# Kernel optimization log

Hardware: AMD Instinct MI355X
Metric: run time of the kernel (lower is better)

Reference implementation:

```python
import jax, jax.numpy as jnp
import numpy as np

N = 100000
E = 1600000
IN_FT = 128
OUT_FT = 128
SELF_LOOP_FILL = 3.0


def setup_inputs() -> dict:
    key = jax.random.key(0)
    k1, k2, k3, k4 = jax.random.split(key, 4)
    seq = jax.random.normal(k1, (N, IN_FT), dtype=jnp.float32)
    edge_index = jax.random.randint(k2, (2, E), 0, N, dtype=jnp.int64)
    edge_weight = jax.random.uniform(k3, (E,), dtype=jnp.float32)
    # xavier_uniform for Linear(in_ft, out_ft): W shape [out_ft, in_ft]
    limit = float(np.sqrt(6.0 / (IN_FT + OUT_FT)))
    W = jax.random.uniform(k4, (OUT_FT, IN_FT), dtype=jnp.float32, minval=-limit, maxval=limit)
    return {"seq": seq, "edge_weight": edge_weight, "W": W, "edge_index": edge_index}


def reference(seq, edge_weight, W, edge_index):
    n = seq.shape[0]
    # dropout with drop_prob=0.0 is identity; fc_1: x = seq @ W^T
    x = seq @ W.T  # [N, out_ft]
    # add self loops with fill_value=3.0
    loops = jnp.arange(n, dtype=edge_index.dtype)
    row = jnp.concatenate([edge_index[0], loops])
    col = jnp.concatenate([edge_index[1], loops])
    w = jnp.concatenate([edge_weight, jnp.full((n,), SELF_LOOP_FILL, dtype=edge_weight.dtype)])
    # symmetric normalization: deg^-1/2 [row] * w * deg^-1/2 [col]
    deg = jax.ops.segment_sum(w, row, num_segments=n)
    deg_inv_sqrt = jnp.where(deg > 0, jax.lax.rsqrt(deg), jnp.zeros_like(deg))
    norm = deg_inv_sqrt[row] * w * deg_inv_sqrt[col]
    # sparse aggregation: out[r] += norm_e * x[c]
    out = jax.ops.segment_sum(norm[:, None] * x[col], row, num_segments=n)
    return jax.nn.relu(out)
```

## Files before the change

kernel.cpp:

```cpp
#include <hip/hip_runtime.h>


#define TPB 256
#define NBROWS 256
#define BCAP 4608
#define RCAP 48
#define EPB 8192

typedef __attribute__((ext_vector_type(8))) short s16x8;
typedef __attribute__((ext_vector_type(4))) float f32x4;

__global__ void k_init(int* __restrict__ cursor, int m) {
    int i = blockIdx.x * TPB + threadIdx.x;
    if (i < m) cursor[i] = 0;
}

__global__ __launch_bounds__(TPB) void k_partition(const int* __restrict__ ei,
                                                   const float* __restrict__ ew,
                                                   int* __restrict__ cursor,
                                                   int2* __restrict__ part,
                                                   int e, int nb) {
    __shared__ int hist[512];
    __shared__ int chunk[512];
    int t = threadIdx.x;
    hist[t] = 0; hist[t + 256] = 0;
    chunk[t] = 0; chunk[t + 256] = 0;
    __syncthreads();

    long base = (long)blockIdx.x * EPB;
    for (int j = 0; j < 32; ++j) {
        long idx = base + j * 256 + t;
        if (idx < e) atomicAdd(&hist[ei[idx] >> 8], 1);
    }
    __syncthreads();
    for (int b = t; b < nb; b += TPB) {
        int h = hist[b];
        chunk[b] = (h > 0) ? atomicAdd(&cursor[b * 16], h) : 0;
    }
    __syncthreads();
    hist[t] = 0; hist[t + 256] = 0;
    __syncthreads();
    for (int j = 0; j < 32; ++j) {
        long idx = base + j * 256 + t;
        if (idx < e) {
            int r = ei[idx];
            int c = ei[e + idx];
            float w = ew[idx];
            int b = r >> 8;
            int rank = atomicAdd(&hist[b], 1);
            int dst = chunk[b] + rank;
            if (dst < BCAP)
                part[(long)b * BCAP + dst] =
                    make_int2(((r & 255) << 17) | c, __float_as_int(w));
        }
    }
}

__global__ __launch_bounds__(TPB) void k_build(const int2* __restrict__ part,
                                               const int* __restrict__ cursor,
                                               unsigned* __restrict__ slotsG,
                                               int* __restrict__ cnt,
                                               float* __restrict__ dis, int n) {
    __shared__ unsigned lslot[NBROWS * RCAP];
    __shared__ int rowcnt[NBROWS];
    int b = blockIdx.x, t = threadIdx.x;
    rowcnt[t] = 0;
    for (int j = t; j < NBROWS * RCAP; j += TPB) lslot[j] = 0;
    __syncthreads();

    int m = cursor[b * 16]; if (m > BCAP) m = BCAP;
    for (int i = t; i < m; i += TPB) {
        int2 en = part[(long)b * BCAP + i];
        int rl = ((unsigned)en.x) >> 17;
        int c  = en.x & 0x1FFFF;
        float w = __int_as_float(en.y);
        int pos = atomicAdd(&rowcnt[rl], 1);
        if (pos < RCAP) {
            int q = (int)(w * 32768.0f);
            if (q > 32767) q = 32767;
            lslot[rl * RCAP + pos] = ((unsigned)q << 17) | (unsigned)c;
        }
    }
    __syncthreads();

    int node = b * NBROWS + t;
    if (node < n) {
        int rc = rowcnt[t]; if (rc > RCAP) rc = RCAP;
        float s = 0.0f;
        for (int k = 0; k < rc; ++k)
            s += ((float)(lslot[t * RCAP + k] >> 17) + 0.5f) * (1.0f / 32768.0f);
        dis[node] = rsqrtf(3.0f + s);
        cnt[node] = rc;
    }
    for (int j = t; j < NBROWS * RCAP; j += TPB)
        slotsG[(long)b * (NBROWS * RCAP) + j] = lslot[j];
}

__device__ inline unsigned bf16rne(float x) {
    unsigned u = __float_as_uint(x);
    u += 0x7FFF + ((u >> 16) & 1);
    return u >> 16;
}

__global__ __launch_bounds__(TPB) void k_prescale(const float* __restrict__ seq,
                                                  const float* __restrict__ dis,
                                                  unsigned* __restrict__ xb, long npairs) {
    long p = (long)blockIdx.x * TPB + threadIdx.x;
    if (p >= npairs) return;
    float d = dis[p >> 6];
    float2 s = ((const float2*)seq)[p];
    xb[p] = bf16rne(d * s.x) | (bf16rne(d * s.y) << 16);
}

__global__ __launch_bounds__(TPB) void k_gather(const unsigned* __restrict__ xb,
                                                const unsigned* __restrict__ slotsG,
                                                const int* __restrict__ cnt,
                                                const float* __restrict__ dis,
                                                float* __restrict__ y, int n) {
    int wave = threadIdx.x >> 6, lane = threadIdx.x & 63;
    int node = blockIdx.x * 4 + wave;
    if (node >= n) return;

    int m = cnt[node];
    float di = dis[node];

    unsigned s_l = (lane < RCAP) ? slotsG[(long)node * RCAP + lane] : 0u;
    int   c_l = (lane < m) ? (int)(s_l & 0x1FFFF) : 0;
    if (c_l > n - 1) c_l = n - 1;
    float v_l = (lane < m) ? ((float)(s_l >> 17) + 0.5f) * (1.0f / 32768.0f) : 0.0f;

    unsigned u = xb[(long)node * 64 + lane];
    float2 acc;
    acc.x = 3.0f * __uint_as_float(u << 16);
    acc.y = 3.0f * __uint_as_float(u & 0xFFFF0000u);

#pragma unroll 4
    for (int p = 0; p < m; ++p) {
        int   c = __shfl(c_l, p);
        float v = __shfl(v_l, p);
        unsigned xv = xb[(long)c * 64 + lane];
        acc.x = fmaf(v, __uint_as_float(xv << 16), acc.x);
        acc.y = fmaf(v, __uint_as_float(xv & 0xFFFF0000u), acc.y);
    }

    ((float2*)(y + (long)node * 128))[lane] = make_float2(di * acc.x, di * acc.y);
}

__global__ __launch_bounds__(TPB) void k_gemm(float* __restrict__ y,
                                              const float* __restrict__ W, int n) {
    __shared__ short wlds[128 * 128];
    __shared__ short ylds[128 * 128];
    int t = threadIdx.x;
    long base = (long)blockIdx.x * 128;

#pragma unroll
    for (int i = 0; i < 8; ++i) {
        int G = i * 256 + t;
        int j = G >> 4, g = G & 15;
        const float* src = W + j * 128 + g * 8;
        float4 f0 = *(const float4*)src;
        float4 f1 = *(const float4*)(src + 4);
        union { s16x8 s; uint4 u; } pk;
        pk.u.x = bf16rne(f0.x) | (bf16rne(f0.y) << 16);
        pk.u.y = bf16rne(f0.z) | (bf16rne(f0.w) << 16);
        pk.u.z = bf16rne(f1.x) | (bf16rne(f1.y) << 16);
        pk.u.w = bf16rne(f1.z) | (bf16rne(f1.w) << 16);
        *(s16x8*)&wlds[j * 128 + ((g ^ (j & 15)) << 3)] = pk.s;
    }
#pragma unroll
    for (int i = 0; i < 8; ++i) {
        int G = i * 256 + t;
        int r = G >> 4, g = G & 15;
        long gr = base + r; if (gr >= n) gr = n - 1;
        const float* src = y + gr * 128 + g * 8;
        float4 f0 = *(const float4*)src;
        float4 f1 = *(const float4*)(src + 4);
        union { s16x8 s; uint4 u; } pk;
        pk.u.x = bf16rne(f0.x) | (bf16rne(f0.y) << 16);
        pk.u.y = bf16rne(f0.z) | (bf16rne(f0.w) << 16);
        pk.u.z = bf16rne(f1.x) | (bf16rne(f1.y) << 16);
        pk.u.w = bf16rne(f1.z) | (bf16rne(f1.w) << 16);
        *(s16x8*)&ylds[r * 128 + ((g ^ (r & 15)) << 3)] = pk.s;
    }
    __syncthreads();

    int wave = t >> 6, lane = t & 63;
    int quad = lane >> 4, l15 = lane & 15;

    f32x4 acc[2][8];
#pragma unroll
    for (int h = 0; h < 2; ++h)
#pragma unroll
        for (int ct = 0; ct < 8; ++ct)
            acc[h][ct] = (f32x4){0.0f, 0.0f, 0.0f, 0.0f};

    int r0 = wave * 32 + l15;
    int r1 = wave * 32 + 16 + l15;

#pragma unroll
    for (int kc = 0; kc < 4; ++kc) {
        int gA = kc * 4 + quad;
        s16x8 a0 = *(const s16x8*)&ylds[r0 * 128 + ((gA ^ l15) << 3)];
        s16x8 a1 = *(const s16x8*)&ylds[r1 * 128 + ((gA ^ l15) << 3)];
#pragma unroll
        for (int ct = 0; ct < 8; ++ct) {
            int j = ct * 16 + l15;
            s16x8 b = *(const s16x8*)&wlds[j * 128 + ((gA ^ l15) << 3)];
            acc[0][ct] = __builtin_amdgcn_mfma_f32_16x16x32_bf16(a0, b, acc[0][ct], 0, 0, 0);
            acc[1][ct] = __builtin_amdgcn_mfma_f32_16x16x32_bf16(a1, b, acc[1][ct], 0, 0, 0);
        }
    }

#pragma unroll
    for (int h = 0; h < 2; ++h) {
        long rloc = wave * 32 + h * 16 + quad * 4;
#pragma unroll
        for (int i = 0; i < 4; ++i) {
            long gr = base + rloc + i;
            if (gr < n) {
                float* dst = y + gr * 128 + l15;
#pragma unroll
                for (int ct = 0; ct < 8; ++ct)
                    dst[ct * 16] = fmaxf(acc[h][ct][i], 0.0f);
            }
        }
    }
}

extern "C" void kernel_launch(void* const* d_in, const int* in_sizes, int n_in,
                              void* d_out, int out_size, void* d_ws, size_t ws_size,
                              hipStream_t stream) {
    const float* seq = (const float*)d_in[0];
    const float* ew  = (const float*)d_in[1];
    const float* W   = (const float*)d_in[2];
    const int*   ei  = (const int*)d_in[3];
    float* out = (float*)d_out;

    int n = in_sizes[0] / 128;
    int e = in_sizes[1];
    int nb = (n + NBROWS - 1) / NBROWS;

    char* w8 = (char*)d_ws;
    unsigned* xb   = (unsigned*)w8;
    size_t off = (size_t)n * 64 * 4;
    int2* part     = (int2*)(w8 + off);
    off += (size_t)nb * BCAP * 8;
    unsigned* slotsG = (unsigned*)(w8 + off);
    off += (size_t)nb * NBROWS * RCAP * 4;
    int* cursor    = (int*)(w8 + off);
    off += (size_t)nb * 16 * 4;
    int* cnt       = (int*)(w8 + off);
    off += (size_t)n * 4;
    float* dis     = (float*)(w8 + off);

    long npairs = (long)n * 64;

    k_init     <<<(nb * 16 + TPB - 1) / TPB, TPB, 0, stream>>>(cursor, nb * 16);
    k_partition<<<(e + EPB - 1) / EPB, TPB, 0, stream>>>(ei, ew, cursor, part, e, nb);
    k_build    <<<nb, TPB, 0, stream>>>(part, cursor, slotsG, cnt, dis, n);
    k_prescale <<<(int)((npairs + TPB - 1) / TPB), TPB, 0, stream>>>(seq, dis, xb, npairs);
    k_gather   <<<(n + 3) / 4, TPB, 0, stream>>>(xb, slotsG, cnt, dis, out, n);
    k_gemm     <<<(n + 127) / 128, TPB, 0, stream>>>(out, W, n);
}
```

Measured before the change: 293.5 us.

## Slice feature matrix into column panels and gather eight edges per wave

The prescaled bf16 feature matrix is stored as eight column slices of 16 features, each slice contiguous across nodes, so that each gather block touches only one slice and that slice's working set fits better in cache. Each wave now handles 16 nodes serially and processes eight edges at once, with each lane group of 8 loading a 32-byte piece, followed by a cross-lane shuffle reduction. Degree and count are packed into one float2 load, and the partition kernel uses smaller edge chunks to launch more blocks. The cost is eight passes over the slot lists, plus reduction shuffles and partly idle lanes for short rows.

```diff
diff --git a/kernel.cpp b/kernel.cpp
--- a/kernel.cpp
+++ b/kernel.cpp
@@ -5,7 +5,7 @@
 #define NBROWS 256
 #define BCAP 4608
 #define RCAP 48
-#define EPB 8192
+#define EPB 2048
 
 typedef __attribute__((ext_vector_type(8))) short s16x8;
 typedef __attribute__((ext_vector_type(4))) float f32x4;
@@ -28,7 +28,7 @@
     __syncthreads();
 
     long base = (long)blockIdx.x * EPB;
-    for (int j = 0; j < 32; ++j) {
+    for (int j = 0; j < EPB / 256; ++j) {
         long idx = base + j * 256 + t;
         if (idx < e) atomicAdd(&hist[ei[idx] >> 8], 1);
     }
@@ -40,7 +40,7 @@
     __syncthreads();
     hist[t] = 0; hist[t + 256] = 0;
     __syncthreads();
-    for (int j = 0; j < 32; ++j) {
+    for (int j = 0; j < EPB / 256; ++j) {
         long idx = base + j * 256 + t;
         if (idx < e) {
             int r = ei[idx];
@@ -59,7 +59,7 @@
 __global__ __launch_bounds__(TPB) void k_build(const int2* __restrict__ part,
                                                const int* __restrict__ cursor,
                                                unsigned* __restrict__ slotsG,
-                                               int* __restrict__ cnt,
+                                               float2* __restrict__ dc,
                                                float* __restrict__ dis, int n) {
     __shared__ unsigned lslot[NBROWS * RCAP];
     __shared__ int rowcnt[NBROWS];
@@ -89,8 +89,9 @@
         float s = 0.0f;
         for (int k = 0; k < rc; ++k)
             s += ((float)(lslot[t * RCAP + k] >> 17) + 0.5f) * (1.0f / 32768.0f);
-        dis[node] = rsqrtf(3.0f + s);
-        cnt[node] = rc;
+        float di = rsqrtf(3.0f + s);
+        dis[node] = di;
+        dc[node] = make_float2(di, __int_as_float(rc));
     }
     for (int j = t; j < NBROWS * RCAP; j += TPB)
         slotsG[(long)b * (NBROWS * RCAP) + j] = lslot[j];
@@ -104,46 +105,69 @@
 
 __global__ __launch_bounds__(TPB) void k_prescale(const float* __restrict__ seq,
                                                   const float* __restrict__ dis,
-                                                  unsigned* __restrict__ xb, long npairs) {
+                                                  unsigned* __restrict__ xb, int n) {
     long p = (long)blockIdx.x * TPB + threadIdx.x;
-    if (p >= npairs) return;
-    float d = dis[p >> 6];
+    if (p >= (long)n * 64) return;
+    int node = (int)(p >> 6), fp = (int)(p & 63);
+    float d = dis[node];
     float2 s = ((const float2*)seq)[p];
-    xb[p] = bf16rne(d * s.x) | (bf16rne(d * s.y) << 16);
+    xb[((long)(fp >> 3) * n + node) * 8 + (fp & 7)] =
+        bf16rne(d * s.x) | (bf16rne(d * s.y) << 16);
 }
 
 __global__ __launch_bounds__(TPB) void k_gather(const unsigned* __restrict__ xb,
                                                 const unsigned* __restrict__ slotsG,
-                                                const int* __restrict__ cnt,
-                                                const float* __restrict__ dis,
+                                                const float2* __restrict__ dc,
                                                 float* __restrict__ y, int n) {
+    int slice = blockIdx.x & 7;
+    int chunk = blockIdx.x >> 3;
     int wave = threadIdx.x >> 6, lane = threadIdx.x & 63;
-    int node = blockIdx.x * 4 + wave;
-    if (node >= n) return;
-
-    int m = cnt[node];
-    float di = dis[node];
-
-    unsigned s_l = (lane < RCAP) ? slotsG[(long)node * RCAP + lane] : 0u;
-    int   c_l = (lane < m) ? (int)(s_l & 0x1FFFF) : 0;
-    if (c_l > n - 1) c_l = n - 1;
-    float v_l = (lane < m) ? ((float)(s_l >> 17) + 0.5f) * (1.0f / 32768.0f) : 0.0f;
-
-    unsigned u = xb[(long)node * 64 + lane];
-    float2 acc;
-    acc.x = 3.0f * __uint_as_float(u << 16);
-    acc.y = 3.0f * __uint_as_float(u & 0xFFFF0000u);
-
-#pragma unroll 4
-    for (int p = 0; p < m; ++p) {
-        int   c = __shfl(c_l, p);
-        float v = __shfl(v_l, p);
-        unsigned xv = xb[(long)c * 64 + lane];
-        acc.x = fmaf(v, __uint_as_float(xv << 16), acc.x);
-        acc.y = fmaf(v, __uint_as_float(xv & 0xFFFF0000u), acc.y);
-    }
-
-    ((float2*)(y + (long)node * 128))[lane] = make_float2(di * acc.x, di * acc.y);
+    int e8 = lane >> 3, d = lane & 7;
+    const unsigned* xs = xb + (long)slice * n * 8;
+
+    int node0 = chunk * 64 + wave * 16;
+#pragma unroll 1
+    for (int i = 0; i < 16; ++i) {
+        int node = node0 + i;
+        if (node >= n) break;
+        float2 dcv = dc[node];
+        float di = dcv.x;
+        int m = __float_as_int(dcv.y);
+
+        unsigned s_l = (lane < m) ? slotsG[(long)node * RCAP + lane] : 0u;
+
+        float2 acc = {0.0f, 0.0f};
+        if (e8 == 0) {
+            unsigned u = xs[(long)node * 8 + d];
+            acc.x = 3.0f * __uint_as_float(u << 16);
+            acc.y = 3.0f * __uint_as_float(u & 0xFFFF0000u);
+        }
+
+#pragma unroll 2
+        for (int p = 0; p < m; p += 8) {
+            int idx = p + e8;
+            unsigned sl = __shfl(s_l, idx);
+            int c = sl & 0x1FFFF;
+            if (c > n - 1) c = n - 1;
+            float v = (idx < m)
+                ? fmaf((float)(sl >> 17), 3.0517578125e-05f, 1.52587890625e-05f)
+                : 0.0f;
+            unsigned xv = xs[(long)c * 8 + d];
+            acc.x = fmaf(v, __uint_as_float(xv << 16), acc.x);
+            acc.y = fmaf(v, __uint_as_float(xv & 0xFFFF0000u), acc.y);
+        }
+
+        acc.x += __shfl_xor(acc.x, 8);
+        acc.y += __shfl_xor(acc.y, 8);
+        acc.x += __shfl_xor(acc.x, 16);
+        acc.y += __shfl_xor(acc.y, 16);
+        acc.x += __shfl_xor(acc.x, 32);
+        acc.y += __shfl_xor(acc.y, 32);
+
+        if (e8 == 0)
+            ((float2*)(y + (long)node * 128 + slice * 16))[d] =
+                make_float2(di * acc.x, di * acc.y);
+    }
 }
 
 __global__ __launch_bounds__(TPB) void k_gemm(float* __restrict__ y,
@@ -249,16 +273,14 @@
     off += (size_t)nb * NBROWS * RCAP * 4;
     int* cursor    = (int*)(w8 + off);
     off += (size_t)nb * 16 * 4;
-    int* cnt       = (int*)(w8 + off);
-    off += (size_t)n * 4;
+    float2* dc     = (float2*)(w8 + off);
+    off += (size_t)n * 8;
     float* dis     = (float*)(w8 + off);
-
-    long npairs = (long)n * 64;
 
     k_init     <<<(nb * 16 + TPB - 1) / TPB, TPB, 0, stream>>>(cursor, nb * 16);
     k_partition<<<(e + EPB - 1) / EPB, TPB, 0, stream>>>(ei, ew, cursor, part, e, nb);
-    k_build    <<<nb, TPB, 0, stream>>>(part, cursor, slotsG, cnt, dis, n);
-    k_prescale <<<(int)((npairs + TPB - 1) / TPB), TPB, 0, stream>>>(seq, dis, xb, npairs);
-    k_gather   <<<(n + 3) / 4, TPB, 0, stream>>>(xb, slotsG, cnt, dis, out, n);
+    k_build    <<<nb, TPB, 0, stream>>>(part, cursor, slotsG, dc, dis, n);
+    k_prescale <<<(int)(((long)n * 64 + TPB - 1) / TPB), TPB, 0, stream>>>(seq, dis, xb, n);
+    k_gather   <<<((n + 63) / 64) * 8, TPB, 0, stream>>>(xb, slotsG, dc, out, n);
     k_gemm     <<<(n + 127) / 128, TPB, 0, stream>>>(out, W, n);
 }
```

After: 390.4 us. 1.33x slower.
